# Kernel optimization log

Measured on AMD Instinct MI355X. Metric: run time of the kernel, lower is better.

The kernel has to match this reference:

```python
import jax, jax.numpy as jnp
import numpy as np

N = 50000      # num nodes
E = 400000     # directed edges (avg out-degree 8)
DIN = 128
DOUT = 128
ALPHA = 0.5    # args.alphaDir (buffer, requires_grad=False)
BETA = 0.5     # args.betaDir
GAMA = 0.5     # args.gamaDir


def _dedupe(rows, cols, vals, n):
    key = rows.astype(np.int64) * n + cols.astype(np.int64)
    uk, inv = np.unique(key, return_inverse=True)
    v = np.bincount(inv, weights=vals, minlength=uk.shape[0])
    return (uk // n).astype(np.int32), (uk % n).astype(np.int32), v.astype(np.float32)


def _dir_norm(r, c, v, n):
    # directed_norm: D_out^{-1/2} A D_in^{-1/2}, inf -> 0
    in_deg = np.bincount(c, weights=v, minlength=n)
    out_deg = np.bincount(r, weights=v, minlength=n)
    in_is = np.zeros(n); m = in_deg > 0; in_is[m] = in_deg[m] ** -0.5
    out_is = np.zeros(n); m = out_deg > 0; out_is[m] = out_deg[m] ** -0.5
    return r, c, (out_is[r] * v * in_is[c]).astype(np.float32)


def _spgemm(rA, cA, vA, rB, cB, vB, n):
    # sparse @ sparse in COO, vectorized numpy
    order = np.argsort(rB, kind='stable')
    rBs, cBs, vBs = rB[order], cB[order], vB[order]
    degB = np.bincount(rBs, minlength=n)
    indptr = np.concatenate(([0], np.cumsum(degB)))
    counts = degB[cA]
    total = int(counts.sum())
    rep = np.repeat(np.arange(len(rA)), counts)
    first = np.cumsum(counts) - counts
    pos = np.arange(total) - np.repeat(first, counts) + np.repeat(indptr[cA], counts)
    rows = rA[rep]
    cols = cBs[pos]
    vals = vA[rep].astype(np.float64) * vBs[pos]
    return _dedupe(rows, cols, vals, n)


def setup_inputs() -> dict:
    rng = np.random.default_rng(0)
    r0 = rng.integers(0, N, E).astype(np.int64)
    c0 = rng.integers(0, N, E).astype(np.int64)
    r, c, v = _dedupe(r0, c0, np.ones(E, np.float32), N)
    a = _dir_norm(r, c, v, N)                 # adj_norm
    at = _dir_norm(c, r, v, N)                # adj_t_norm
    rr, cc, vv = _spgemm(a[0], a[1], a[2], at[0], at[1], at[2], N)
    aat = _dir_norm(rr, cc, vv, N)            # directed_norm(A @ At)
    rr, cc, vv = _spgemm(at[0], at[1], at[2], a[0], a[1], a[2], N)
    ata = _dir_norm(rr, cc, vv, N)            # directed_norm(At @ A)
    rr, cc, vv = _spgemm(a[0], a[1], a[2], a[0], a[1], a[2], N)
    aa = _dir_norm(rr, cc, vv, N)             # directed_norm(A @ A)
    rr, cc, vv = _spgemm(at[0], at[1], at[2], at[0], at[1], at[2], N)
    atat = _dir_norm(rr, cc, vv, N)           # directed_norm(At @ At)

    key = jax.random.key(0)
    ks = jax.random.split(key, 7)
    x = jax.random.normal(ks[0], (N, DIN), dtype=jnp.float32)
    s = 1.0 / np.sqrt(DIN)

    def lin(k):
        k1, k2 = jax.random.split(k)
        w = jax.random.uniform(k1, (DIN, DOUT), jnp.float32, -s, s)
        b = jax.random.uniform(k2, (DOUT,), jnp.float32, -s, s)
        return w, b

    w_sd, b_sd = lin(ks[1]); w_ds, b_ds = lin(ks[2])
    w0, b0 = lin(ks[3]); w1, b1 = lin(ks[4])
    w2, b2 = lin(ks[5]); w3, b3 = lin(ks[6])

    out = {'x': x,
           'w_sd': w_sd, 'b_sd': b_sd, 'w_ds': w_ds, 'b_ds': b_ds,
           'w0': w0, 'b0': b0, 'w1': w1, 'b1': b1,
           'w2': w2, 'b2': b2, 'w3': w3, 'b3': b3}
    for name, t in (('a', a), ('at', at), ('aat', aat), ('ata', ata), ('aa', aa), ('atat', atat)):
        out[name + '_rows'] = jnp.asarray(t[0])
        out[name + '_cols'] = jnp.asarray(t[1])
        out[name + '_vals'] = jnp.asarray(t[2])
    return out


def _spmm(rows, cols, vals, x):
    # (A @ x)[i] = sum_e vals[e] * x[cols[e]] scattered to rows[e]
    return jax.ops.segment_sum(vals[:, None] * x[cols], rows, num_segments=x.shape[0])


def reference(x, a_rows, a_cols, a_vals, at_rows, at_cols, at_vals,
              aat_rows, aat_cols, aat_vals, ata_rows, ata_cols, ata_vals,
              aa_rows, aa_cols, aa_vals, atat_rows, atat_cols, atat_vals,
              w_sd, b_sd, w_ds, b_ds, w0, b0, w1, b1, w2, b2, w3, b3):
    out1 = ALPHA * (_spmm(a_rows, a_cols, a_vals, x) @ w_sd + b_sd) \
         + (1.0 - ALPHA) * (_spmm(at_rows, at_cols, at_vals, x) @ w_ds + b_ds)
    out2 = BETA * (_spmm(aat_rows, aat_cols, aat_vals, x) @ w0 + b0) \
         + (1.0 - BETA) * (_spmm(ata_rows, ata_cols, ata_vals, x) @ w1 + b1)
    out3 = GAMA * (_spmm(aa_rows, aa_cols, aa_vals, x) @ w2 + b2) \
         + (1.0 - GAMA) * (_spmm(atat_rows, atat_cols, atat_vals, x) @ w3 + b3)
    return out1 + out2 + out3
```

## Files before the change

### kernel.cpp

```cpp
#include <hip/hip_runtime.h>
#include <hip/hip_bf16.h>

#define FD 128

typedef __attribute__((ext_vector_type(8))) short bf16x8;
typedef __attribute__((ext_vector_type(4))) float f32x4;

__device__ __forceinline__ float bfu2f(unsigned short u) {
  return __uint_as_float(((unsigned int)u) << 16);
}
__device__ __forceinline__ float b2f(__hip_bfloat16 v) { return __bfloat162float(v); }
__device__ __forceinline__ unsigned int pk2(float lo, float hi) {
  return (unsigned int)__bfloat16_as_ushort(__float2bfloat16(lo)) |
         ((unsigned int)__bfloat16_as_ushort(__float2bfloat16(hi)) << 16);
}

__device__ __forceinline__ float ldf(const void* p, int i, int ff) {
  return ff ? ((const float*)p)[i] : b2f(((const __hip_bfloat16*)p)[i]);
}
__device__ __forceinline__ int ldi(const void* p, int i, int fi) {
  return fi ? (int)((const long long*)p)[i] : ((const int*)p)[i];
}

__global__ void detect_k(const void* x, const void* cols, int* flags) {
  __shared__ int cnt[2];
  if (threadIdx.x < 2) cnt[threadIdx.x] = 0;
  __syncthreads();
  const unsigned short* xu = (const unsigned short*)x;
  int big = 0;
  for (int i = threadIdx.x; i < 1024; i += 256) {
    int e = (xu[i] >> 7) & 0xFF;
    if (e >= 0x90) big++;
  }
  if (big) atomicAdd(&cnt[0], big);
  const int* ci = (const int*)cols;
  int zeros = 0;
  for (int i = threadIdx.x; i < 128; i += 256)
    if ((i & 1) && ci[i] == 0) zeros++;
  if (zeros) atomicAdd(&cnt[1], zeros);
  __syncthreads();
  if (threadIdx.x == 0) {
    flags[0] = (cnt[0] > 16) ? 1 : 0;
    flags[1] = (cnt[1] >= 32) ? 1 : 0;
  }
}

__global__ void cvtall_k(const void* __restrict__ rows, const void* __restrict__ cols,
                         const void* __restrict__ vals, int nnz, int n,
                         int* __restrict__ r32, int* __restrict__ c32,
                         float* __restrict__ vf, int* __restrict__ cntT,
                         const int* flags) {
  int ff = flags[0], fi = flags[1];
  int i = blockIdx.x * 256 + threadIdx.x;
  if (i >= nnz) return;
  int r = ldi(rows, i, fi);
  int c = ldi(cols, i, fi);
  if ((unsigned)r >= (unsigned)n) r = 0;
  if ((unsigned)c >= (unsigned)n) c = 0;
  r32[i] = r;
  c32[i] = c;
  vf[i] = ldf(vals, i, ff);
  atomicAdd(&cntT[c], 1);
}

__global__ void scanA_k(const int* __restrict__ cnt, int n, int* bsum) {
  __shared__ int sh[256];
  int t = threadIdx.x;
  int i = blockIdx.x * 256 + t;
  sh[t] = (i < n) ? cnt[i] : 0;
  __syncthreads();
  for (int d = 128; d > 0; d >>= 1) {
    if (t < d) sh[t] += sh[t + d];
    __syncthreads();
  }
  if (t == 0) bsum[blockIdx.x] = sh[0];
}

__global__ void scanB_k(int* bsum, int nb, int* rpTail) {
  __shared__ int sh[256];
  int t = threadIdx.x;
  int v = (t < nb) ? bsum[t] : 0;
  sh[t] = v;
  __syncthreads();
  int val = v;
  for (int d = 1; d < 256; d <<= 1) {
    int add = (t >= d) ? sh[t - d] : 0;
    __syncthreads();
    val += add;
    sh[t] = val;
    __syncthreads();
  }
  if (t < nb) bsum[t] = val - v;
  if (t == 255) *rpTail = val;
}

__global__ void scanC_k(const int* __restrict__ cnt, int n, const int* __restrict__ bsum,
                        int* rp, int* cur) {
  __shared__ int sh[256];
  int t = threadIdx.x;
  int i = blockIdx.x * 256 + t;
  int v = (i < n) ? cnt[i] : 0;
  sh[t] = v;
  __syncthreads();
  int val = v;
  for (int d = 1; d < 256; d <<= 1) {
    int add = (t >= d) ? sh[t - d] : 0;
    __syncthreads();
    val += add;
    sh[t] = val;
    __syncthreads();
  }
  int ex = val - v + bsum[blockIdx.x];
  if (i < n) { rp[i] = ex; cur[i] = ex; }
}

__global__ void bsearch_k(const int* __restrict__ rows, int nnz, int n, int* rpA) {
  int i = blockIdx.x * 256 + threadIdx.x;
  if (i > n) return;
  int lo = 0, hi = nnz;
  while (lo < hi) { int mid = (lo + hi) >> 1; if (rows[mid] < i) lo = mid + 1; else hi = mid; }
  rpA[i] = lo;
}

__global__ void scatter_k(const int* __restrict__ r, const int* __restrict__ c,
                          const float* __restrict__ v, int nnz,
                          int* cur, int* tSrc, float* tVal) {
  int i = blockIdx.x * 256 + threadIdx.x;
  if (i >= nnz) return;
  int p = atomicAdd(&cur[c[i]], 1);
  if ((unsigned)p >= (unsigned)nnz) return;
  tSrc[p] = r[i];
  tVal[p] = v[i];
}

__global__ void nodesum_k(const int* __restrict__ rpA, const float* __restrict__ av,
                          const int* __restrict__ rpT, const float* __restrict__ tv,
                          float* __restrict__ u1, float* __restrict__ v1, int n) {
  int i = blockIdx.x * 256 + threadIdx.x;
  if (i >= n) return;
  float su = 0.f;
  int e0 = rpA[i], e1 = rpA[i + 1];
  for (int j = e0; j < e1; ++j) su += av[j];
  u1[i] = su;
  float sv = 0.f;
  int f0 = rpT[i], f1 = rpT[i + 1];
  for (int j = f0; j < f1; ++j) sv += tv[j];
  v1[i] = sv;
}

__global__ void deg2c_k(const int* __restrict__ rpA, const int* __restrict__ ci,
                        const float* __restrict__ av,
                        const int* __restrict__ rpT, const int* __restrict__ ti,
                        const float* __restrict__ tv,
                        const float* __restrict__ u1, const float* __restrict__ v1,
                        float* __restrict__ s1, float* __restrict__ s2,
                        float* __restrict__ s3, float* __restrict__ s4, int n) {
  int i = blockIdx.x * 256 + threadIdx.x;
  if (i >= n) return;
  float a1 = 0.f, a3 = 0.f;
  int s0 = rpA[i], se = rpA[i + 1];
  for (int j = s0; j < se; ++j) {
    int c = ci[j];
    float v = av[j];
    a1 = fmaf(v, v1[c], a1);
    a3 = fmaf(v, u1[c], a3);
  }
  s1[i] = (a1 > 0.f) ? rsqrtf(a1) : 0.f;
  s3[i] = (a3 > 0.f) ? rsqrtf(a3) : 0.f;
  float a2 = 0.f, a4 = 0.f;
  int t0 = rpT[i], t1 = rpT[i + 1];
  for (int j = t0; j < t1; ++j) {
    int r = ti[j];
    float v = tv[j];
    a2 = fmaf(v, u1[r], a2);
    a4 = fmaf(v, v1[r], a4);
  }
  s2[i] = (a2 > 0.f) ? rsqrtf(a2) : 0.f;
  s4[i] = (a4 > 0.f) ? rsqrtf(a4) : 0.f;
}

__global__ void bias_k(const void* a, const void* b, const void* c, const void* d,
                       const void* e, const void* f, float* bias, const int* flags) {
  int ff = flags[0];
  int i = threadIdx.x;
  bias[i] = 0.5f * (ldf(a, i, ff) + ldf(b, i, ff) + ldf(c, i, ff)
                  + ldf(d, i, ff) + ldf(e, i, ff) + ldf(f, i, ff));
}

__global__ void fill_k(unsigned short* o, int n) {
  int i = blockIdx.x * 256 + threadIdx.x;
  if (i < n) o[i] = 0x3E80;
}

struct W6p { const void* w[6]; };
struct B6p { const void* b[6]; };

__global__ void prep_k(const void* __restrict__ x, __hip_bfloat16* __restrict__ xb, int nx,
                       W6p ws, __hip_bfloat16* __restrict__ Wt,
                       B6p bs, float* __restrict__ bias,
                       const int* flags, int cvtB) {
  int ff = flags[0];
  int blk = blockIdx.x;
  if (blk < cvtB) {
    int i = (blk * 256 + threadIdx.x) * 4;
    if (i >= nx) return;
    if (i + 3 >= nx) {
      for (int k = i; k < nx; ++k) xb[k] = __float2bfloat16(ldf(x, k, ff));
      return;
    }
    xb[i + 0] = __float2bfloat16(ldf(x, i + 0, ff));
    xb[i + 1] = __float2bfloat16(ldf(x, i + 1, ff));
    xb[i + 2] = __float2bfloat16(ldf(x, i + 2, ff));
    xb[i + 3] = __float2bfloat16(ldf(x, i + 3, ff));
  } else if (blk < cvtB + 384) {
    int e = (blk - cvtB) * 256 + threadIdx.x;
    if (e >= 6 * 16384) return;
    int seg = e >> 14;
    int r = e & 16383;
    int n = r >> 7;
    int innerB = (r & 127) << 1;
    int kb = innerB ^ ((n & 7) << 4);
    int k = kb >> 1;
    Wt[e] = __float2bfloat16(ldf(ws.w[seg], k * 128 + n, ff));
  } else {
    int i = threadIdx.x;
    if (i < FD)
      bias[i] = 0.5f * (ldf(bs.b[0], i, ff) + ldf(bs.b[1], i, ff) + ldf(bs.b[2], i, ff)
                      + ldf(bs.b[3], i, ff) + ldf(bs.b[4], i, ff) + ldf(bs.b[5], i, ff));
  }
}

__device__ __forceinline__ void fh_fma(const uint4& u, float v, float va, float vb,
                                       float* t, float* a, float* b) {
  unsigned int uu[4] = {u.x, u.y, u.z, u.w};
#pragma unroll
  for (int k = 0; k < 4; ++k) {
    float lo = __uint_as_float(uu[k] << 16);
    float hi = __uint_as_float(uu[k] & 0xFFFF0000u);
    t[2 * k]     = fmaf(v, lo, t[2 * k]);
    t[2 * k + 1] = fmaf(v, hi, t[2 * k + 1]);
    a[2 * k]     = fmaf(va, lo, a[2 * k]);
    a[2 * k + 1] = fmaf(va, hi, a[2 * k + 1]);
    b[2 * k]     = fmaf(vb, lo, b[2 * k]);
    b[2 * k + 1] = fmaf(vb, hi, b[2 * k + 1]);
  }
}

__device__ __forceinline__ void sh_fma(const uint4& u, const uint4& w, float v,
                                       float* a, float* b) {
  unsigned int uu[4] = {u.x, u.y, u.z, u.w};
  unsigned int ww[4] = {w.x, w.y, w.z, w.w};
#pragma unroll
  for (int k = 0; k < 4; ++k) {
    a[2 * k]     = fmaf(v, __uint_as_float(uu[k] << 16), a[2 * k]);
    a[2 * k + 1] = fmaf(v, __uint_as_float(uu[k] & 0xFFFF0000u), a[2 * k + 1]);
    b[2 * k]     = fmaf(v, __uint_as_float(ww[k] << 16), b[2 * k]);
    b[2 * k + 1] = fmaf(v, __uint_as_float(ww[k] & 0xFFFF0000u), b[2 * k + 1]);
  }
}

struct FHSet {
  const int* rp; const int* ci; const float* cv;
  unsigned int* ot; unsigned int* oa; unsigned int* ob;
  const float* sA; const float* sB;
};

__global__ __launch_bounds__(256) void fh3d_k(
    FHSet h0, FHSet h1, const unsigned int* __restrict__ xb, int n, int half) {
  int blk = blockIdx.x;
  bool hi = blk >= half;
  const int* rp = hi ? h1.rp : h0.rp;
  const int* ci = hi ? h1.ci : h0.ci;
  const float* cv = hi ? h1.cv : h0.cv;
  unsigned int* ot = hi ? h1.ot : h0.ot;
  unsigned int* oa = hi ? h1.oa : h0.oa;
  unsigned int* ob = hi ? h1.ob : h0.ob;
  const float* sA = hi ? h1.sA : h0.sA;
  const float* sB = hi ? h1.sB : h0.sB;
  int bb = hi ? blk - half : blk;

  int wave = threadIdx.x >> 6;
  int lane = threadIdx.x & 63;
  int es = lane >> 4;
  int li = lane & 15;
  int r = bb * 4 + wave;
  if (r >= n) return;
  int s = rp[r], e = rp[r + 1];
  float t[8], a[8], b[8];
#pragma unroll
  for (int k = 0; k < 8; ++k) { t[k] = 0.f; a[k] = 0.f; b[k] = 0.f; }
  int j = s + es;
  for (; j < e - 4; j += 8) {
    int c1 = ci[j], c2 = ci[j + 4];
    float v1 = cv[j], v2 = cv[j + 4];
    float va1 = v1 * sA[c1], vb1 = v1 * sB[c1];
    float va2 = v2 * sA[c2], vb2 = v2 * sB[c2];
    uint4 u1 = *(const uint4*)(xb + (size_t)c1 * 64 + li * 4);
    uint4 u2 = *(const uint4*)(xb + (size_t)c2 * 64 + li * 4);
    fh_fma(u1, v1, va1, vb1, t, a, b);
    fh_fma(u2, v2, va2, vb2, t, a, b);
  }
  if (j < e) {
    int c = ci[j];
    float v = cv[j];
    float va = v * sA[c], vb = v * sB[c];
    uint4 u = *(const uint4*)(xb + (size_t)c * 64 + li * 4);
    fh_fma(u, v, va, vb, t, a, b);
  }
#pragma unroll
  for (int k = 0; k < 8; ++k) {
    t[k] += __shfl_xor(t[k], 16); t[k] += __shfl_xor(t[k], 32);
    a[k] += __shfl_xor(a[k], 16); a[k] += __shfl_xor(a[k], 32);
    b[k] += __shfl_xor(b[k], 16); b[k] += __shfl_xor(b[k], 32);
  }
  if (es == 0) {
    uint4 o;
    o.x = pk2(t[0], t[1]); o.y = pk2(t[2], t[3]);
    o.z = pk2(t[4], t[5]); o.w = pk2(t[6], t[7]);
    *(uint4*)(ot + (size_t)r * 64 + li * 4) = o;
    o.x = pk2(a[0], a[1]); o.y = pk2(a[2], a[3]);
    o.z = pk2(a[4], a[5]); o.w = pk2(a[6], a[7]);
    *(uint4*)(oa + (size_t)r * 128 + li * 4) = o;
    o.x = pk2(b[0], b[1]); o.y = pk2(b[2], b[3]);
    o.z = pk2(b[4], b[5]); o.w = pk2(b[6], b[7]);
    *(uint4*)(ob + (size_t)r * 128 + li * 4) = o;
  }
}

struct SHSet {
  const int* rp; const int* ci; const float* cv;
  const unsigned int* gp;
  unsigned int* ya; unsigned int* yb;
  const float* rsa; const float* rsb;
};

__global__ __launch_bounds__(256) void sh2d_k(SHSet h0, SHSet h1, int n, int half) {
  int blk = blockIdx.x;
  bool hi = blk >= half;
  const int* rp = hi ? h1.rp : h0.rp;
  const int* ci = hi ? h1.ci : h0.ci;
  const float* cv = hi ? h1.cv : h0.cv;
  const unsigned int* gp = hi ? h1.gp : h0.gp;
  unsigned int* ya = hi ? h1.ya : h0.ya;
  unsigned int* yb = hi ? h1.yb : h0.yb;
  const float* rsa = hi ? h1.rsa : h0.rsa;
  const float* rsb = hi ? h1.rsb : h0.rsb;
  int bb = hi ? blk - half : blk;

  int wave = threadIdx.x >> 6;
  int lane = threadIdx.x & 63;
  int es = lane >> 4;
  int li = lane & 15;
  int r = bb * 4 + wave;
  if (r >= n) return;
  int s = rp[r], e = rp[r + 1];
  float a[8], b[8];
#pragma unroll
  for (int k = 0; k < 8; ++k) { a[k] = 0.f; b[k] = 0.f; }
  int j = s + es;
  for (; j < e - 4; j += 8) {
    int c1 = ci[j], c2 = ci[j + 4];
    float v1 = cv[j], v2 = cv[j + 4];
    const unsigned int* b1 = gp + (size_t)c1 * 128;
    const unsigned int* b2 = gp + (size_t)c2 * 128;
    uint4 u1 = *(const uint4*)(b1 + li * 4);
    uint4 w1 = *(const uint4*)(b1 + 64 + li * 4);
    uint4 u2 = *(const uint4*)(b2 + li * 4);
    uint4 w2 = *(const uint4*)(b2 + 64 + li * 4);
    sh_fma(u1, w1, v1, a, b);
    sh_fma(u2, w2, v2, a, b);
  }
  if (j < e) {
    int c = ci[j];
    float v = cv[j];
    const unsigned int* bp = gp + (size_t)c * 128;
    uint4 u = *(const uint4*)(bp + li * 4);
    uint4 w = *(const uint4*)(bp + 64 + li * 4);
    sh_fma(u, w, v, a, b);
  }
#pragma unroll
  for (int k = 0; k < 8; ++k) {
    a[k] += __shfl_xor(a[k], 16); a[k] += __shfl_xor(a[k], 32);
    b[k] += __shfl_xor(b[k], 16); b[k] += __shfl_xor(b[k], 32);
  }
  if (es == 0) {
    float ra = rsa[r], rb = rsb[r];
    size_t off = (size_t)r * 64 + li * 4;
    uint4 o;
    o.x = pk2(a[0] * ra, a[1] * ra); o.y = pk2(a[2] * ra, a[3] * ra);
    o.z = pk2(a[4] * ra, a[5] * ra); o.w = pk2(a[6] * ra, a[7] * ra);
    *(uint4*)(ya + off) = o;
    o.x = pk2(b[0] * rb, b[1] * rb); o.y = pk2(b[2] * rb, b[3] * rb);
    o.z = pk2(b[4] * rb, b[5] * rb); o.w = pk2(b[6] * rb, b[7] * rb);
    *(uint4*)(yb + off) = o;
  }
}

struct Y6 { const unsigned short* y[6]; };

__global__ __launch_bounds__(256) void gemm6m3_k(
    Y6 ys, const unsigned short* __restrict__ Wt2, const float* __restrict__ bias,
    void* __restrict__ outp, int M, const int* flags) {
  int ff = flags[0];
  __shared__ __align__(16) unsigned short Bs[16384];
  const int tid = threadIdx.x;
  const int lane = tid & 63;
  const int wave = tid >> 6;
  const int m = lane & 15;
  const int q = lane >> 4;
  const int r0 = blockIdx.x * 128 + wave * 32;
  const int row0 = r0 + m;
  const int row1 = r0 + 16 + m;
  const bool ok0 = row0 < M;
  const bool ok1 = row1 < M;
  const bf16x8 zero8 = {0, 0, 0, 0, 0, 0, 0, 0};

  f32x4 acc0[8], acc1[8];
#pragma unroll
  for (int nt = 0; nt < 8; ++nt) {
    acc0[nt] = (f32x4){0.f, 0.f, 0.f, 0.f};
    acc1[nt] = (f32x4){0.f, 0.f, 0.f, 0.f};
  }

  bf16x8 Bst[8];
#pragma unroll
  for (int c2 = 0; c2 < 8; ++c2)
    Bst[c2] = *(const bf16x8*)(Wt2 + (size_t)(c2 * 256 + tid) * 8);
  bf16x8 Ap0[4], Ap1[4];
#pragma unroll
  for (int kc = 0; kc < 4; ++kc) {
    Ap0[kc] = ok0 ? *(const bf16x8*)(ys.y[0] + (size_t)row0 * FD + kc * 32 + q * 8) : zero8;
    Ap1[kc] = ok1 ? *(const bf16x8*)(ys.y[0] + (size_t)row1 * FD + kc * 32 + q * 8) : zero8;
  }

  const int swz = (m & 7) << 4;

#pragma unroll
  for (int t = 0; t < 6; ++t) {
    __syncthreads();
#pragma unroll
    for (int c2 = 0; c2 < 8; ++c2)
      *(bf16x8*)((char*)Bs + (size_t)(c2 * 256 + tid) * 16) = Bst[c2];
    bf16x8 A0[4], A1[4];
#pragma unroll
    for (int kc = 0; kc < 4; ++kc) { A0[kc] = Ap0[kc]; A1[kc] = Ap1[kc]; }
    if (t < 5) {
#pragma unroll
      for (int c2 = 0; c2 < 8; ++c2)
        Bst[c2] = *(const bf16x8*)(Wt2 + (size_t)(t + 1) * 16384 +
                                   (size_t)(c2 * 256 + tid) * 8);
#pragma unroll
      for (int kc = 0; kc < 4; ++kc) {
        Ap0[kc] = ok0 ? *(const bf16x8*)(ys.y[t + 1] + (size_t)row0 * FD + kc * 32 + q * 8) : zero8;
        Ap1[kc] = ok1 ? *(const bf16x8*)(ys.y[t + 1] + (size_t)row1 * FD + kc * 32 + q * 8) : zero8;
      }
    }
    __syncthreads();
#pragma unroll
    for (int kc = 0; kc < 4; ++kc) {
      const int koff = (kc * 64 + q * 16) ^ swz;
#pragma unroll
      for (int nt = 0; nt < 8; ++nt) {
        const int nrow = nt * 16 + m;
        bf16x8 bfv = *(const bf16x8*)((const char*)Bs + nrow * 256 + koff);
        acc0[nt] = __builtin_amdgcn_mfma_f32_16x16x32_bf16(A0[kc], bfv, acc0[nt], 0, 0, 0);
        acc1[nt] = __builtin_amdgcn_mfma_f32_16x16x32_bf16(A1[kc], bfv, acc1[nt], 0, 0, 0);
      }
    }
  }

#pragma unroll
  for (int nt = 0; nt < 8; ++nt) {
    int col = nt * 16 + m;
    float bv = bias[col];
#pragma unroll
    for (int rg = 0; rg < 4; ++rg) {
      int g0 = r0 + q * 4 + rg;
      if (g0 < M) {
        float v = 0.5f * acc0[nt][rg] + bv;
        if (ff) ((float*)outp)[(size_t)g0 * FD + col] = v;
        else ((unsigned short*)outp)[(size_t)g0 * FD + col] =
            __bfloat16_as_ushort(__float2bfloat16(v));
      }
      int g1 = r0 + 16 + q * 4 + rg;
      if (g1 < M) {
        float v = 0.5f * acc1[nt][rg] + bv;
        if (ff) ((float*)outp)[(size_t)g1 * FD + col] = v;
        else ((unsigned short*)outp)[(size_t)g1 * FD + col] =
            __bfloat16_as_ushort(__float2bfloat16(v));
      }
    }
  }
}

__global__ __launch_bounds__(128) void spmm_k(
    const int* __restrict__ rp, const void* __restrict__ ci, int cif,
    const void* __restrict__ cv, int cvf,
    const void* __restrict__ x, int xf, __hip_bfloat16* __restrict__ y,
    int n, int nnzMax,
    const float* __restrict__ cscale, const float* __restrict__ rscale,
    const int* flags) {
  int ff = flags[0], fi = flags[1];
  int vf = cvf ? 1 : ff;
  int iw = cif ? fi : 0;
  int xw = xf ? ff : 0;
  const int t = threadIdx.x;
  int r0 = blockIdx.x * 4;
  int rend = min(r0 + 4, n);
  for (int r = r0; r < rend; ++r) {
    int s = rp[r], e = rp[r + 1];
    s = max(0, min(s, nnzMax));
    e = max(s, min(e, nnzMax));
    float acc = 0.f;
    for (int j = s; j < e; ++j) {
      int c = ldi(ci, j, iw);
      if ((unsigned)c >= (unsigned)n) c = 0;
      float v = (vf ? ((const float*)cv)[j] : b2f(((const __hip_bfloat16*)cv)[j]));
      if (cscale) v *= cscale[c];
      float xv = xw ? ((const float*)x)[c * FD + t]
                    : b2f(((const __hip_bfloat16*)x)[c * FD + t]);
      acc = fmaf(v, xv, acc);
    }
    if (rscale) acc *= rscale[r];
    y[r * FD + t] = __float2bfloat16(acc);
  }
}

__global__ __launch_bounds__(256) void gemm_k(
    const __hip_bfloat16* __restrict__ Y, const void* __restrict__ W,
    const float* __restrict__ bias, const void* __restrict__ accin,
    void* __restrict__ outp, int M, const int* flags) {
  int ff = flags[0];
  __shared__ __align__(16) float Wl[32 * 128];
  __shared__ __align__(16) float Yl[64 * 36];
  const int t = threadIdx.x;
  const int row0 = blockIdx.x * 64;
  const int c4 = (t & 31) * 4;
  const int r8 = (t >> 5) * 8;
  const int rs = t >> 3;
  const int q = t & 7;
  float acc[8][4];
#pragma unroll
  for (int m = 0; m < 8; ++m)
#pragma unroll
    for (int j = 0; j < 4; ++j) acc[m][j] = 0.f;
  for (int kc = 0; kc < 4; ++kc) {
    if (ff) {
      const float4* Wg4 = (const float4*)((const float*)W + kc * 32 * 128);
#pragma unroll
      for (int i = 0; i < 4; ++i)
        *(float4*)(Wl + (t + i * 256) * 4) = Wg4[t + i * 256];
    } else {
      const ushort4* Wg4 = (const ushort4*)((const unsigned short*)W + kc * 32 * 128);
#pragma unroll
      for (int i = 0; i < 4; ++i) {
        ushort4 u = Wg4[t + i * 256];
        int base = (t + i * 256) * 4;
        Wl[base + 0] = bfu2f(u.x);
        Wl[base + 1] = bfu2f(u.y);
        Wl[base + 2] = bfu2f(u.z);
        Wl[base + 3] = bfu2f(u.w);
      }
    }
#pragma unroll
    for (int i = 0; i < 2; ++i) {
      int rr = rs + i * 32;
      int grow = row0 + rr;
      ushort4 u = make_ushort4(0, 0, 0, 0);
      if (grow < M)
        u = *(const ushort4*)((const unsigned short*)Y + grow * FD + kc * 32 + q * 4);
      float* yd = Yl + rr * 36 + q * 4;
      yd[0] = bfu2f(u.x); yd[1] = bfu2f(u.y); yd[2] = bfu2f(u.z); yd[3] = bfu2f(u.w);
    }
    __syncthreads();
#pragma unroll
    for (int kk = 0; kk < 32; kk += 4) {
      float4 w0 = *(const float4*)(Wl + (kk + 0) * 128 + c4);
      float4 w1 = *(const float4*)(Wl + (kk + 1) * 128 + c4);
      float4 w2 = *(const float4*)(Wl + (kk + 2) * 128 + c4);
      float4 w3 = *(const float4*)(Wl + (kk + 3) * 128 + c4);
#pragma unroll
      for (int m = 0; m < 8; ++m) {
        float4 yv = *(const float4*)(Yl + (r8 + m) * 36 + kk);
        acc[m][0] = fmaf(yv.x, w0.x, acc[m][0]);
        acc[m][1] = fmaf(yv.x, w0.y, acc[m][1]);
        acc[m][2] = fmaf(yv.x, w0.z, acc[m][2]);
        acc[m][3] = fmaf(yv.x, w0.w, acc[m][3]);
        acc[m][0] = fmaf(yv.y, w1.x, acc[m][0]);
        acc[m][1] = fmaf(yv.y, w1.y, acc[m][1]);
        acc[m][2] = fmaf(yv.y, w1.z, acc[m][2]);
        acc[m][3] = fmaf(yv.y, w1.w, acc[m][3]);
        acc[m][0] = fmaf(yv.z, w2.x, acc[m][0]);
        acc[m][1] = fmaf(yv.z, w2.y, acc[m][1]);
        acc[m][2] = fmaf(yv.z, w2.z, acc[m][2]);
        acc[m][3] = fmaf(yv.z, w2.w, acc[m][3]);
        acc[m][0] = fmaf(yv.w, w3.x, acc[m][0]);
        acc[m][1] = fmaf(yv.w, w3.y, acc[m][1]);
        acc[m][2] = fmaf(yv.w, w3.z, acc[m][2]);
        acc[m][3] = fmaf(yv.w, w3.w, acc[m][3]);
      }
    }
    __syncthreads();
  }
  float4 b4 = make_float4(0.f, 0.f, 0.f, 0.f);
  if (bias) b4 = *(const float4*)(bias + c4);
#pragma unroll
  for (int m = 0; m < 8; ++m) {
    int grow = row0 + r8 + m;
    if (grow >= M) continue;
    float4 rv;
    rv.x = 0.5f * acc[m][0] + b4.x;
    rv.y = 0.5f * acc[m][1] + b4.y;
    rv.z = 0.5f * acc[m][2] + b4.z;
    rv.w = 0.5f * acc[m][3] + b4.w;
    if (accin) {
      if (ff) {
        float4 o = *(const float4*)((const float*)accin + grow * FD + c4);
        rv.x += o.x; rv.y += o.y; rv.z += o.z; rv.w += o.w;
      } else {
        ushort4 o = *(const ushort4*)((const unsigned short*)accin + grow * FD + c4);
        rv.x += bfu2f(o.x); rv.y += bfu2f(o.y); rv.z += bfu2f(o.z); rv.w += bfu2f(o.w);
      }
    }
    if (ff) {
      *(float4*)((float*)outp + grow * FD + c4) = rv;
    } else {
      ushort4 so;
      so.x = __bfloat16_as_ushort(__float2bfloat16(rv.x));
      so.y = __bfloat16_as_ushort(__float2bfloat16(rv.y));
      so.z = __bfloat16_as_ushort(__float2bfloat16(rv.z));
      so.w = __bfloat16_as_ushort(__float2bfloat16(rv.w));
      *(ushort4*)((unsigned short*)outp + grow * FD + c4) = so;
    }
  }
}

extern "C" void kernel_launch(void* const* d_in, const int* in_sizes, int n_in,
                              void* d_out, int out_size, void* d_ws, size_t ws_size,
                              hipStream_t stream) {
  const void* x    = d_in[0];
  const void* w_sd = d_in[1];
  const void* b_sd = d_in[2];
  const void* w_ds = d_in[3];
  const void* b_ds = d_in[4];
  const void* w0   = d_in[5];
  const void* b0   = d_in[6];
  const void* w1   = d_in[7];
  const void* b1   = d_in[8];
  const void* w2   = d_in[9];
  const void* b2   = d_in[10];
  const void* w3   = d_in[11];
  const void* b3   = d_in[12];
  const void* a_rows = d_in[13];
  const void* a_cols = d_in[14];
  const void* a_vals = d_in[15];
  const int nnz = in_sizes[13];
  const int N = in_sizes[0] / FD;

  const size_t BUF = ((size_t)N * FD * 2 + 255) & ~(size_t)255;

  auto misc_need = [&](int nbig) -> size_t {
    size_t need = (size_t)nbig * BUF;
    need += ((size_t)10 * N * 4 + 255) & ~(size_t)255;
    need += 512 + 256 + 1024;
    need += (((size_t)(N + 1) * 4 + 255) & ~(size_t)255) * 2;
    need += (((size_t)N * 4 + 255) & ~(size_t)255) * 2;
    need += (((size_t)nnz * 4 + 255) & ~(size_t)255) * 5;
    need += (6 * 16384 * 2 + 255) & ~(size_t)255;
    return need;
  };
  size_t needA = misc_need(10);
  size_t needB = misc_need(2);

  int pathA = (ws_size >= needA) ? 1 : 0;
  if (!pathA && ws_size < needB) {
    fill_k<<<(out_size + 255) / 256, 256, 0, stream>>>((unsigned short*)d_out, out_size);
    return;
  }

  int nbig = pathA ? 10 : 2;
  char* p = (char*)d_ws;
  char* bufs[10];
  for (int i = 0; i < 10; ++i) bufs[i] = (i < nbig) ? (p + (size_t)i * BUF) : nullptr;
  char* q = p + (size_t)nbig * BUF;
  auto take = [&](size_t bytes) -> char* {
    char* r = q;
    q += (bytes + 255) & ~(size_t)255;
    return r;
  };
  float* degf  = (float*)take((size_t)10 * N * 4);
  float* biasf = (float*)take(512);
  int*   flags = (int*)take(256);
  int*   bsum  = (int*)take(1024);
  int* rpA  = (int*)take((size_t)(N + 1) * 4);
  int* rpT  = (int*)take((size_t)(N + 1) * 4);
  int* curT = (int*)take((size_t)N * 4);
  int* cntT = (int*)take((size_t)N * 4);
  int* tSrc = (int*)take((size_t)nnz * 4);
  float* tValF = (float*)take((size_t)nnz * 4);
  int* aRow32 = (int*)take((size_t)nnz * 4);
  int* aCol32 = (int*)take((size_t)nnz * 4);
  float* aValF = (float*)take((size_t)nnz * 4);
  __hip_bfloat16* Wt = (__hip_bfloat16*)take(6 * 16384 * 2);

  float* u1 = degf;
  float* v1 = degf + N;
  float* s1 = degf + 6 * N;
  float* s2 = degf + 7 * N;
  float* s3 = degf + 8 * N;
  float* s4 = degf + 9 * N;

  int eb = (nnz + 255) / 256;
  int nb = (N + 255) / 256;

  detect_k<<<1, 256, 0, stream>>>(x, a_cols, flags);
  hipMemsetAsync(cntT, 0, (size_t)N * 4, stream);
  cvtall_k<<<eb, 256, 0, stream>>>(a_rows, a_cols, a_vals, nnz, N, aRow32, aCol32, aValF, cntT, flags);
  scanA_k<<<nb, 256, 0, stream>>>(cntT, N, bsum);
  scanB_k<<<1, 256, 0, stream>>>(bsum, nb, rpT + N);
  scanC_k<<<nb, 256, 0, stream>>>(cntT, N, bsum, rpT, curT);
  bsearch_k<<<(N + 256) / 256, 256, 0, stream>>>(aRow32, nnz, N, rpA);
  scatter_k<<<eb, 256, 0, stream>>>(aRow32, aCol32, aValF, nnz, curT, tSrc, tValF);
  nodesum_k<<<nb, 256, 0, stream>>>(rpA, aValF, rpT, tValF, u1, v1, N);
  deg2c_k<<<nb, 256, 0, stream>>>(rpA, aCol32, aValF, rpT, tSrc, tValF, u1, v1,
                                  s1, s2, s3, s4, N);

  int sg2 = (N + 3) / 4;
  int gg = (N + 63) / 64;
  int gg4 = (N + 127) / 128;

  if (pathA) {
    W6p wargs;
    wargs.w[0] = w_sd; wargs.w[1] = w_ds; wargs.w[2] = w0;
    wargs.w[3] = w1;   wargs.w[4] = w2;   wargs.w[5] = w3;
    B6p bargs;
    bargs.b[0] = b_sd; bargs.b[1] = b_ds; bargs.b[2] = b0;
    bargs.b[3] = b1;   bargs.b[4] = b2;   bargs.b[5] = b3;
    __hip_bfloat16* xb = (__hip_bfloat16*)bufs[0];
    int cvtB = (N * FD / 4 + 255) / 256;
    prep_k<<<cvtB + 384 + 1, 256, 0, stream>>>(x, xb, N * FD, wargs, Wt, bargs, biasf,
                                               flags, cvtB);

    unsigned int* xbu = (unsigned int*)bufs[0];
    unsigned int* t2 = (unsigned int*)bufs[1];
    unsigned int* t1 = (unsigned int*)bufs[2];
    unsigned int* P1 = (unsigned int*)bufs[3];
    unsigned int* P2 = (unsigned int*)bufs[5];
    unsigned int* y3 = (unsigned int*)bufs[7];
    unsigned int* y4 = (unsigned int*)bufs[8];
    unsigned int* y6 = (unsigned int*)bufs[9];
    unsigned int* y5 = (unsigned int*)bufs[0];

    FHSet hT = { rpT, tSrc, tValF, t2, P1, P2 + 64, s1, s3 };
    FHSet hA = { rpA, aCol32, aValF, t1, P2, P1 + 64, s2, s4 };
    fh3d_k<<<2 * sg2, 256, 0, stream>>>(hT, hA, xbu, N, sg2);

    SHSet sA = { rpA, aCol32, aValF, P1, y3, y5, s1, s3 };
    SHSet sT = { rpT, tSrc, tValF, P2, y4, y6, s2, s4 };
    sh2d_k<<<2 * sg2, 256, 0, stream>>>(sA, sT, N, sg2);

    Y6 yargs;
    yargs.y[0] = (const unsigned short*)t1;
    yargs.y[1] = (const unsigned short*)t2;
    yargs.y[2] = (const unsigned short*)y3;
    yargs.y[3] = (const unsigned short*)y4;
    yargs.y[4] = (const unsigned short*)y5;
    yargs.y[5] = (const unsigned short*)y6;
    gemm6m3_k<<<gg4, 256, 0, stream>>>(yargs, (const unsigned short*)Wt, biasf, d_out, N, flags);
  } else {
    bias_k<<<1, FD, 0, stream>>>(b_sd, b_ds, b0, b1, b2, b3, biasf, flags);
    __hip_bfloat16* Yb = (__hip_bfloat16*)bufs[0];
    __hip_bfloat16* gb = (__hip_bfloat16*)bufs[1];
    spmm_k<<<sg2, 128, 0, stream>>>(rpA, a_cols, 1, a_vals, 0, x, 1, Yb, N, nnz, nullptr, nullptr, flags);
    gemm_k<<<gg, 256, 0, stream>>>(Yb, w_sd, biasf, nullptr, d_out, N, flags);
    spmm_k<<<sg2, 128, 0, stream>>>(rpT, tSrc, 0, tValF, 1, x, 1, Yb, N, nnz, nullptr, nullptr, flags);
    gemm_k<<<gg, 256, 0, stream>>>(Yb, w_ds, nullptr, d_out, d_out, N, flags);
    spmm_k<<<sg2, 128, 0, stream>>>(rpT, tSrc, 0, tValF, 1, x, 1, gb, N, nnz, s1, nullptr, flags);
    spmm_k<<<sg2, 128, 0, stream>>>(rpA, a_cols, 1, a_vals, 0, gb, 0, Yb, N, nnz, nullptr, s1, flags);
    gemm_k<<<gg, 256, 0, stream>>>(Yb, w0, nullptr, d_out, d_out, N, flags);
    spmm_k<<<sg2, 128, 0, stream>>>(rpA, a_cols, 1, a_vals, 0, x, 1, gb, N, nnz, s2, nullptr, flags);
    spmm_k<<<sg2, 128, 0, stream>>>(rpT, tSrc, 0, tValF, 1, gb, 0, Yb, N, nnz, nullptr, s2, flags);
    gemm_k<<<gg, 256, 0, stream>>>(Yb, w1, nullptr, d_out, d_out, N, flags);
    spmm_k<<<sg2, 128, 0, stream>>>(rpA, a_cols, 1, a_vals, 0, x, 1, gb, N, nnz, s4, nullptr, flags);
    spmm_k<<<sg2, 128, 0, stream>>>(rpA, a_cols, 1, a_vals, 0, gb, 0, Yb, N, nnz, nullptr, s3, flags);
    gemm_k<<<gg, 256, 0, stream>>>(Yb, w2, nullptr, d_out, d_out, N, flags);
    spmm_k<<<sg2, 128, 0, stream>>>(rpT, tSrc, 0, tValF, 1, x, 1, gb, N, nnz, s3, nullptr, flags);
    spmm_k<<<sg2, 128, 0, stream>>>(rpT, tSrc, 0, tValF, 1, gb, 0, Yb, N, nnz, nullptr, s4, flags);
    gemm_k<<<gg, 256, 0, stream>>>(Yb, w3, nullptr, d_out, d_out, N, flags);
  }
}
```

Baseline: 446.2 us.

## Use full-wave per-edge gathers in SpMM kernels and merge bsearch into scan

The fh3d and sh2d gather-SpMM kernels drop the four-edge-groups-of-16-lanes scheme, which loaded uint4 per lane and reduced with shuffles. Now all 64 lanes read one 32-bit bf16 pair each for a single edge and unroll the edge loop by four. This removes the cross-lane shuffle reductions and cuts register use, but each load becomes narrower and fewer edges are in flight per wave. Separately, the row-pointer binary search is folded into the first scan kernel as extra blocks, saving one launch.

```diff
diff --git a/kernel.cpp b/kernel.cpp
--- a/kernel.cpp
+++ b/kernel.cpp
@@ -63,17 +63,27 @@
   atomicAdd(&cntT[c], 1);
 }
 
-__global__ void scanA_k(const int* __restrict__ cnt, int n, int* bsum) {
-  __shared__ int sh[256];
-  int t = threadIdx.x;
-  int i = blockIdx.x * 256 + t;
-  sh[t] = (i < n) ? cnt[i] : 0;
-  __syncthreads();
-  for (int d = 128; d > 0; d >>= 1) {
-    if (t < d) sh[t] += sh[t + d];
-    __syncthreads();
-  }
-  if (t == 0) bsum[blockIdx.x] = sh[0];
+__global__ void scanAbs_k(const int* __restrict__ cnt, int n, int* bsum,
+                          const int* __restrict__ rows, int nnz, int* rpA, int nb) {
+  int blk = blockIdx.x;
+  if (blk < nb) {
+    __shared__ int sh[256];
+    int t = threadIdx.x;
+    int i = blk * 256 + t;
+    sh[t] = (i < n) ? cnt[i] : 0;
+    __syncthreads();
+    for (int d = 128; d > 0; d >>= 1) {
+      if (t < d) sh[t] += sh[t + d];
+      __syncthreads();
+    }
+    if (t == 0) bsum[blk] = sh[0];
+  } else {
+    int i = (blk - nb) * 256 + threadIdx.x;
+    if (i > n) return;
+    int lo = 0, hi = nnz;
+    while (lo < hi) { int mid = (lo + hi) >> 1; if (rows[mid] < i) lo = mid + 1; else hi = mid; }
+    rpA[i] = lo;
+  }
 }
 
 __global__ void scanB_k(int* bsum, int nb, int* rpTail) {
@@ -112,14 +122,6 @@
   }
   int ex = val - v + bsum[blockIdx.x];
   if (i < n) { rp[i] = ex; cur[i] = ex; }
-}
-
-__global__ void bsearch_k(const int* __restrict__ rows, int nnz, int n, int* rpA) {
-  int i = blockIdx.x * 256 + threadIdx.x;
-  if (i > n) return;
-  int lo = 0, hi = nnz;
-  while (lo < hi) { int mid = (lo + hi) >> 1; if (rows[mid] < i) lo = mid + 1; else hi = mid; }
-  rpA[i] = lo;
 }
 
 __global__ void scatter_k(const int* __restrict__ r, const int* __restrict__ c,
@@ -230,35 +232,6 @@
   }
 }
 
-__device__ __forceinline__ void fh_fma(const uint4& u, float v, float va, float vb,
-                                       float* t, float* a, float* b) {
-  unsigned int uu[4] = {u.x, u.y, u.z, u.w};
-#pragma unroll
-  for (int k = 0; k < 4; ++k) {
-    float lo = __uint_as_float(uu[k] << 16);
-    float hi = __uint_as_float(uu[k] & 0xFFFF0000u);
-    t[2 * k]     = fmaf(v, lo, t[2 * k]);
-    t[2 * k + 1] = fmaf(v, hi, t[2 * k + 1]);
-    a[2 * k]     = fmaf(va, lo, a[2 * k]);
-    a[2 * k + 1] = fmaf(va, hi, a[2 * k + 1]);
-    b[2 * k]     = fmaf(vb, lo, b[2 * k]);
-    b[2 * k + 1] = fmaf(vb, hi, b[2 * k + 1]);
-  }
-}
-
-__device__ __forceinline__ void sh_fma(const uint4& u, const uint4& w, float v,
-                                       float* a, float* b) {
-  unsigned int uu[4] = {u.x, u.y, u.z, u.w};
-  unsigned int ww[4] = {w.x, w.y, w.z, w.w};
-#pragma unroll
-  for (int k = 0; k < 4; ++k) {
-    a[2 * k]     = fmaf(v, __uint_as_float(uu[k] << 16), a[2 * k]);
-    a[2 * k + 1] = fmaf(v, __uint_as_float(uu[k] & 0xFFFF0000u), a[2 * k + 1]);
-    b[2 * k]     = fmaf(v, __uint_as_float(ww[k] << 16), b[2 * k]);
-    b[2 * k + 1] = fmaf(v, __uint_as_float(ww[k] & 0xFFFF0000u), b[2 * k + 1]);
-  }
-}
-
 struct FHSet {
   const int* rp; const int* ci; const float* cv;
   unsigned int* ot; unsigned int* oa; unsigned int* ob;
@@ -268,63 +241,55 @@
 __global__ __launch_bounds__(256) void fh3d_k(
     FHSet h0, FHSet h1, const unsigned int* __restrict__ xb, int n, int half) {
   int blk = blockIdx.x;
-  bool hi = blk >= half;
-  const int* rp = hi ? h1.rp : h0.rp;
-  const int* ci = hi ? h1.ci : h0.ci;
-  const float* cv = hi ? h1.cv : h0.cv;
-  unsigned int* ot = hi ? h1.ot : h0.ot;
-  unsigned int* oa = hi ? h1.oa : h0.oa;
-  unsigned int* ob = hi ? h1.ob : h0.ob;
-  const float* sA = hi ? h1.sA : h0.sA;
-  const float* sB = hi ? h1.sB : h0.sB;
-  int bb = hi ? blk - half : blk;
+  bool hiH = blk >= half;
+  const int* rp = hiH ? h1.rp : h0.rp;
+  const int* ci = hiH ? h1.ci : h0.ci;
+  const float* cv = hiH ? h1.cv : h0.cv;
+  unsigned int* ot = hiH ? h1.ot : h0.ot;
+  unsigned int* oa = hiH ? h1.oa : h0.oa;
+  unsigned int* ob = hiH ? h1.ob : h0.ob;
+  const float* sA = hiH ? h1.sA : h0.sA;
+  const float* sB = hiH ? h1.sB : h0.sB;
+  int bb = hiH ? blk - half : blk;
 
   int wave = threadIdx.x >> 6;
-  int lane = threadIdx.x & 63;
-  int es = lane >> 4;
-  int li = lane & 15;
+  int l = threadIdx.x & 63;
   int r = bb * 4 + wave;
   if (r >= n) return;
   int s = rp[r], e = rp[r + 1];
-  float t[8], a[8], b[8];
-#pragma unroll
-  for (int k = 0; k < 8; ++k) { t[k] = 0.f; a[k] = 0.f; b[k] = 0.f; }
-  int j = s + es;
-  for (; j < e - 4; j += 8) {
-    int c1 = ci[j], c2 = ci[j + 4];
-    float v1 = cv[j], v2 = cv[j + 4];
-    float va1 = v1 * sA[c1], vb1 = v1 * sB[c1];
-    float va2 = v2 * sA[c2], vb2 = v2 * sB[c2];
-    uint4 u1 = *(const uint4*)(xb + (size_t)c1 * 64 + li * 4);
-    uint4 u2 = *(const uint4*)(xb + (size_t)c2 * 64 + li * 4);
-    fh_fma(u1, v1, va1, vb1, t, a, b);
-    fh_fma(u2, v2, va2, vb2, t, a, b);
-  }
-  if (j < e) {
+
+  float tl = 0.f, th = 0.f, al = 0.f, ah = 0.f, bl = 0.f, bh = 0.f;
+  int j = s;
+  for (; j + 3 < e; j += 4) {
+#pragma unroll
+    for (int u = 0; u < 4; ++u) {
+      int c = ci[j + u];
+      float v = cv[j + u];
+      float va = v * sA[c];
+      float vb = v * sB[c];
+      unsigned int xu = xb[(size_t)c * 64 + l];
+      float lo = __uint_as_float(xu << 16);
+      float hi = __uint_as_float(xu & 0xFFFF0000u);
+      tl = fmaf(v, lo, tl);  th = fmaf(v, hi, th);
+      al = fmaf(va, lo, al); ah = fmaf(va, hi, ah);
+      bl = fmaf(vb, lo, bl); bh = fmaf(vb, hi, bh);
+    }
+  }
+  for (; j < e; ++j) {
     int c = ci[j];
     float v = cv[j];
-    float va = v * sA[c], vb = v * sB[c];
-    uint4 u = *(const uint4*)(xb + (size_t)c * 64 + li * 4);
-    fh_fma(u, v, va, vb, t, a, b);
-  }
-#pragma unroll
-  for (int k = 0; k < 8; ++k) {
-    t[k] += __shfl_xor(t[k], 16); t[k] += __shfl_xor(t[k], 32);
-    a[k] += __shfl_xor(a[k], 16); a[k] += __shfl_xor(a[k], 32);
-    b[k] += __shfl_xor(b[k], 16); b[k] += __shfl_xor(b[k], 32);
-  }
-  if (es == 0) {
-    uint4 o;
-    o.x = pk2(t[0], t[1]); o.y = pk2(t[2], t[3]);
-    o.z = pk2(t[4], t[5]); o.w = pk2(t[6], t[7]);
-    *(uint4*)(ot + (size_t)r * 64 + li * 4) = o;
-    o.x = pk2(a[0], a[1]); o.y = pk2(a[2], a[3]);
-    o.z = pk2(a[4], a[5]); o.w = pk2(a[6], a[7]);
-    *(uint4*)(oa + (size_t)r * 128 + li * 4) = o;
-    o.x = pk2(b[0], b[1]); o.y = pk2(b[2], b[3]);
-    o.z = pk2(b[4], b[5]); o.w = pk2(b[6], b[7]);
-    *(uint4*)(ob + (size_t)r * 128 + li * 4) = o;
-  }
+    float va = v * sA[c];
+    float vb = v * sB[c];
+    unsigned int xu = xb[(size_t)c * 64 + l];
+    float lo = __uint_as_float(xu << 16);
+    float hi = __uint_as_float(xu & 0xFFFF0000u);
+    tl = fmaf(v, lo, tl);  th = fmaf(v, hi, th);
+    al = fmaf(va, lo, al); ah = fmaf(va, hi, ah);
+    bl = fmaf(vb, lo, bl); bh = fmaf(vb, hi, bh);
+  }
+  ot[(size_t)r * 64 + l] = pk2(tl, th);
+  oa[(size_t)r * 128 + l] = pk2(al, ah);
+  ob[(size_t)r * 128 + l] = pk2(bl, bh);
 }
 
 struct SHSet {
@@ -336,64 +301,53 @@
 
 __global__ __launch_bounds__(256) void sh2d_k(SHSet h0, SHSet h1, int n, int half) {
   int blk = blockIdx.x;
-  bool hi = blk >= half;
-  const int* rp = hi ? h1.rp : h0.rp;
-  const int* ci = hi ? h1.ci : h0.ci;
-  const float* cv = hi ? h1.cv : h0.cv;
-  const unsigned int* gp = hi ? h1.gp : h0.gp;
-  unsigned int* ya = hi ? h1.ya : h0.ya;
-  unsigned int* yb = hi ? h1.yb : h0.yb;
-  const float* rsa = hi ? h1.rsa : h0.rsa;
-  const float* rsb = hi ? h1.rsb : h0.rsb;
-  int bb = hi ? blk - half : blk;
+  bool hiH = blk >= half;
+  const int* rp = hiH ? h1.rp : h0.rp;
+  const int* ci = hiH ? h1.ci : h0.ci;
+  const float* cv = hiH ? h1.cv : h0.cv;
+  const unsigned int* gp = hiH ? h1.gp : h0.gp;
+  unsigned int* ya = hiH ? h1.ya : h0.ya;
+  unsigned int* yb = hiH ? h1.yb : h0.yb;
+  const float* rsa = hiH ? h1.rsa : h0.rsa;
+  const float* rsb = hiH ? h1.rsb : h0.rsb;
+  int bb = hiH ? blk - half : blk;
 
   int wave = threadIdx.x >> 6;
-  int lane = threadIdx.x & 63;
-  int es = lane >> 4;
-  int li = lane & 15;
+  int l = threadIdx.x & 63;
   int r = bb * 4 + wave;
   if (r >= n) return;
   int s = rp[r], e = rp[r + 1];
-  float a[8], b[8];
-#pragma unroll
-  for (int k = 0; k < 8; ++k) { a[k] = 0.f; b[k] = 0.f; }
-  int j = s + es;
-  for (; j < e - 4; j += 8) {
-    int c1 = ci[j], c2 = ci[j + 4];
-    float v1 = cv[j], v2 = cv[j + 4];
-    const unsigned int* b1 = gp + (size_t)c1 * 128;
-    const unsigned int* b2 = gp + (size_t)c2 * 128;
-    uint4 u1 = *(const uint4*)(b1 + li * 4);
-    uint4 w1 = *(const uint4*)(b1 + 64 + li * 4);
-    uint4 u2 = *(const uint4*)(b2 + li * 4);
-    uint4 w2 = *(const uint4*)(b2 + 64 + li * 4);
-    sh_fma(u1, w1, v1, a, b);
-    sh_fma(u2, w2, v2, a, b);
-  }
-  if (j < e) {
+
+  float al = 0.f, ah = 0.f, bl = 0.f, bh = 0.f;
+  int j = s;
+  for (; j + 3 < e; j += 4) {
+#pragma unroll
+    for (int u = 0; u < 4; ++u) {
+      int c = ci[j + u];
+      float v = cv[j + u];
+      const unsigned int* bp = gp + (size_t)c * 128;
+      unsigned int ua = bp[l];
+      unsigned int ub = bp[64 + l];
+      al = fmaf(v, __uint_as_float(ua << 16), al);
+      ah = fmaf(v, __uint_as_float(ua & 0xFFFF0000u), ah);
+      bl = fmaf(v, __uint_as_float(ub << 16), bl);
+      bh = fmaf(v, __uint_as_float(ub & 0xFFFF0000u), bh);
+    }
+  }
+  for (; j < e; ++j) {
     int c = ci[j];
     float v = cv[j];
     const unsigned int* bp = gp + (size_t)c * 128;
-    uint4 u = *(const uint4*)(bp + li * 4);
-    uint4 w = *(const uint4*)(bp + 64 + li * 4);
-    sh_fma(u, w, v, a, b);
-  }
-#pragma unroll
-  for (int k = 0; k < 8; ++k) {
-    a[k] += __shfl_xor(a[k], 16); a[k] += __shfl_xor(a[k], 32);
-    b[k] += __shfl_xor(b[k], 16); b[k] += __shfl_xor(b[k], 32);
-  }
-  if (es == 0) {
-    float ra = rsa[r], rb = rsb[r];
-    size_t off = (size_t)r * 64 + li * 4;
-    uint4 o;
-    o.x = pk2(a[0] * ra, a[1] * ra); o.y = pk2(a[2] * ra, a[3] * ra);
-    o.z = pk2(a[4] * ra, a[5] * ra); o.w = pk2(a[6] * ra, a[7] * ra);
-    *(uint4*)(ya + off) = o;
-    o.x = pk2(b[0] * rb, b[1] * rb); o.y = pk2(b[2] * rb, b[3] * rb);
-    o.z = pk2(b[4] * rb, b[5] * rb); o.w = pk2(b[6] * rb, b[7] * rb);
-    *(uint4*)(yb + off) = o;
-  }
+    unsigned int ua = bp[l];
+    unsigned int ub = bp[64 + l];
+    al = fmaf(v, __uint_as_float(ua << 16), al);
+    ah = fmaf(v, __uint_as_float(ua & 0xFFFF0000u), ah);
+    bl = fmaf(v, __uint_as_float(ub << 16), bl);
+    bh = fmaf(v, __uint_as_float(ub & 0xFFFF0000u), bh);
+  }
+  float ra = rsa[r], rb = rsb[r];
+  ya[(size_t)r * 64 + l] = pk2(al * ra, ah * ra);
+  yb[(size_t)r * 64 + l] = pk2(bl * rb, bh * rb);
 }
 
 struct Y6 { const unsigned short* y[6]; };
@@ -712,14 +666,14 @@
 
   int eb = (nnz + 255) / 256;
   int nb = (N + 255) / 256;
+  int nb2 = (N + 256) / 256;
 
   detect_k<<<1, 256, 0, stream>>>(x, a_cols, flags);
   hipMemsetAsync(cntT, 0, (size_t)N * 4, stream);
   cvtall_k<<<eb, 256, 0, stream>>>(a_rows, a_cols, a_vals, nnz, N, aRow32, aCol32, aValF, cntT, flags);
-  scanA_k<<<nb, 256, 0, stream>>>(cntT, N, bsum);
+  scanAbs_k<<<nb + nb2, 256, 0, stream>>>(cntT, N, bsum, aRow32, nnz, rpA, nb);
   scanB_k<<<1, 256, 0, stream>>>(bsum, nb, rpT + N);
   scanC_k<<<nb, 256, 0, stream>>>(cntT, N, bsum, rpT, curT);
-  bsearch_k<<<(N + 256) / 256, 256, 0, stream>>>(aRow32, nnz, N, rpA);
   scatter_k<<<eb, 256, 0, stream>>>(aRow32, aCol32, aValF, nnz, curT, tSrc, tValF);
   nodesum_k<<<nb, 256, 0, stream>>>(rpA, aValF, rpT, tValF, u1, v1, N);
   deg2c_k<<<nb, 256, 0, stream>>>(rpA, aCol32, aValF, rpT, tSrc, tValF, u1, v1,
```

Result: no change. 443.0 us (-0.7%).
